# Performance work log

Hardware: AMD Instinct MI355X
Metric: run time of the kernel (lower is better)

The kernel has to match this reference:

```python
import jax, jax.numpy as jnp
import numpy as np

B, S, D, H = 2, 2048, 1024, 16
HD = D // H  # head_dim = 64


def setup_inputs() -> dict:
    key = jax.random.key(0)
    k1, k2, k3, k4, k5 = jax.random.split(key, 5)
    x = jax.random.normal(k1, (B, S, D), dtype=jnp.float32)
    # causal additive mask [S, S]: 0 on/below diagonal, -1e9 above
    mask = jnp.where(jnp.tril(jnp.ones((S, S), dtype=bool)), 0.0, -1e9).astype(jnp.float32)
    scale = 1.0 / np.sqrt(D)
    W_qkv = jax.random.normal(k2, (D, 3 * D), dtype=jnp.float32) * scale
    b_qkv = jax.random.normal(k3, (3 * D,), dtype=jnp.float32) * 0.01
    W_o = jax.random.normal(k4, (D, D), dtype=jnp.float32) * scale
    b_o = jax.random.normal(k5, (D,), dtype=jnp.float32) * 0.01
    return {"x": x, "mask": mask, "W_qkv": W_qkv, "b_qkv": b_qkv, "W_o": W_o, "b_o": b_o}


def reference(x, mask, W_qkv, b_qkv, W_o, b_o):
    b, s, d = x.shape
    qkv = x @ W_qkv + b_qkv                         # [B,S,3D]
    qkv = qkv.reshape(b, s, H, 3 * HD).transpose(0, 2, 1, 3)  # [B,H,S,3*HD]
    q, k, v = jnp.split(qkv, 3, axis=-1)            # each [B,H,S,HD]
    scores = jnp.einsum('bhqd,bhkd->bhqk', q, k) / np.sqrt(HD)  # [B,H,S,S]
    scores = scores + mask                           # broadcast [S,S] additive mask
    attn = jax.nn.softmax(scores, axis=-1)
    vals = jnp.einsum('bhqk,bhkd->bhqd', attn, v)    # [B,H,S,HD]
    vals = vals.transpose(0, 2, 1, 3).reshape(b, s, d)
    return vals @ W_o + b_o
```

## Files before the change

kernel.cpp:

```cpp
#include <hip/hip_runtime.h>

#define NB 2
#define NS 2048
#define ND 1024
#define NH 16
#define NHD 64
#define QLD (3 * ND)
#define PADP 72

typedef unsigned short u16;
typedef __attribute__((ext_vector_type(8))) short short8;
typedef __attribute__((ext_vector_type(4))) float f32x4;

__device__ __forceinline__ u16 f2b(float f) {
    unsigned int x = __float_as_uint(f);
    return (u16)((x + 0x7fffu + ((x >> 16) & 1u)) >> 16);
}

__device__ __forceinline__ unsigned int cvtpk(float lo, float hi) {
    unsigned int r;
    asm("v_cvt_pk_bf16_f32 %0, %1, %2" : "=v"(r) : "v"(lo), "v"(hi));
    return r;
}

__device__ __forceinline__ int swz8(int d) {
    return ((d >> 1) ^ (d >> 3)) & 7;
}

__global__ __launch_bounds__(256) void prep(
    const float* __restrict__ x, u16* __restrict__ x_bf,
    const float* __restrict__ Wqkv, u16* __restrict__ WqkvT,
    const float* __restrict__ Wo, u16* __restrict__ WoT)
{
    __shared__ u16 Ts[64 * 72];
    const int bid = blockIdx.x;
    const int t = threadIdx.x;

    if (bid < 2048) {
        const int i = (bid * 256 + t) * 8;
        float4 a = *(const float4*)(x + i);
        float4 b = *(const float4*)(x + i + 4);
        *(ushort4*)(x_bf + i)     = make_ushort4(f2b(a.x), f2b(a.y), f2b(a.z), f2b(a.w));
        *(ushort4*)(x_bf + i + 4) = make_ushort4(f2b(b.x), f2b(b.y), f2b(b.z), f2b(b.w));
        return;
    }

    const float* W; u16* WT; int N, bx, by;
    if (bid < 2048 + 768) {
        const int r = bid - 2048;
        W = Wqkv; WT = WqkvT; N = QLD; bx = r % 48; by = r / 48;
    } else {
        const int r = bid - 2816;
        W = Wo; WT = WoT; N = ND; bx = r & 15; by = r >> 4;
    }
    const int K = ND;
    const int k0 = by << 6, n0 = bx << 6;
    const int rr0 = t >> 4, c = (t & 15) << 2;
    #pragma unroll
    for (int rr = 0; rr < 64; rr += 16) {
        float4 v = *(const float4*)&W[(size_t)(k0 + rr0 + rr) * N + n0 + c];
        Ts[(c + 0) * 72 + rr0 + rr] = f2b(v.x);
        Ts[(c + 1) * 72 + rr0 + rr] = f2b(v.y);
        Ts[(c + 2) * 72 + rr0 + rr] = f2b(v.z);
        Ts[(c + 3) * 72 + rr0 + rr] = f2b(v.w);
    }
    __syncthreads();
    const int n = t >> 2, cc = (t & 3) << 4;
    uint4 a = *(const uint4*)&Ts[n * 72 + cc];
    uint4 b = *(const uint4*)&Ts[n * 72 + cc + 8];
    *(uint4*)&WT[(size_t)(n0 + n) * K + k0 + cc]     = a;
    *(uint4*)&WT[(size_t)(n0 + n) * K + k0 + cc + 8] = b;
}

template <int BN, bool STORE_BF16>
__global__ __launch_bounds__(256) void gemm_mfma(
    const u16* __restrict__ A, const u16* __restrict__ BT,
    const float* __restrict__ bias,
    void* __restrict__ C, int M, int N, int K)
{
    constexpr int AIS = 4;
    constexpr int BIS = BN / 32;
    constexpr int NJ  = BN / 32;
    __shared__ u16 As[128 * 64];
    __shared__ u16 Bs[BN * 64];

    const int tid = threadIdx.x;
    const int wave = tid >> 6, lane = tid & 63;
    const int col = lane & 15, quad = lane >> 4;
    const int wm = wave >> 1, wn = wave & 1;

    const int nwgx = gridDim.x;
    const int wg = blockIdx.y * nwgx + blockIdx.x;
    const int cpx = (nwgx * gridDim.y) >> 3;
    const int swz = (wg & 7) * cpx + (wg >> 3);
    const int row0 = (swz / nwgx) << 7, col0 = (swz % nwgx) * BN;

    f32x4 acc[4][NJ] = {};

    const u16* asrc[AIS];
    u16* adst[AIS];
    #pragma unroll
    for (int is = 0; is < AIS; ++is) {
        const int J = is * 256 + wave * 64 + lane;
        const int m = J >> 3;
        const int q = (J & 7) ^ swz8(m);
        asrc[is] = A + (size_t)(row0 + m) * K + q * 8;
        adst[is] = &As[(size_t)(is * 256 + wave * 64) * 8];
    }
    const u16* bsrc[BIS];
    u16* bdst[BIS];
    #pragma unroll
    for (int is = 0; is < BIS; ++is) {
        const int J = is * 256 + wave * 64 + lane;
        const int m = J >> 3;
        const int q = (J & 7) ^ swz8(m);
        bsrc[is] = BT + (size_t)(col0 + m) * K + q * 8;
        bdst[is] = &Bs[(size_t)(is * 256 + wave * 64) * 8];
    }

    for (int kk = 0; kk < K; kk += 64) {
        __syncthreads();
        #pragma unroll
        for (int is = 0; is < AIS; ++is)
            __builtin_amdgcn_global_load_lds(
                (const __attribute__((address_space(1))) unsigned int*)(asrc[is] + kk),
                (__attribute__((address_space(3))) unsigned int*)adst[is], 16, 0, 0);
        #pragma unroll
        for (int is = 0; is < BIS; ++is)
            __builtin_amdgcn_global_load_lds(
                (const __attribute__((address_space(1))) unsigned int*)(bsrc[is] + kk),
                (__attribute__((address_space(3))) unsigned int*)bdst[is], 16, 0, 0);
        __syncthreads();

        #pragma unroll
        for (int h = 0; h < 2; ++h) {
            short8 af[4], bf[NJ];
            #pragma unroll
            for (int i = 0; i < 4; ++i) {
                const int m = wm * 64 + i * 16 + col;
                af[i] = *(const short8*)&As[(m * 8 + ((4 * h + quad) ^ swz8(m))) * 8];
            }
            #pragma unroll
            for (int j = 0; j < NJ; ++j) {
                const int n = wn * (BN / 2) + j * 16 + col;
                bf[j] = *(const short8*)&Bs[(n * 8 + ((4 * h + quad) ^ swz8(n))) * 8];
            }
            #pragma unroll
            for (int i = 0; i < 4; ++i)
                #pragma unroll
                for (int j = 0; j < NJ; ++j)
                    acc[i][j] = __builtin_amdgcn_mfma_f32_16x16x32_bf16(
                        af[i], bf[j], acc[i][j], 0, 0, 0);
        }
    }

    #pragma unroll
    for (int j = 0; j < NJ; ++j) {
        const int gc = col0 + wn * (BN / 2) + j * 16 + col;
        const float bj = bias[gc];
        #pragma unroll
        for (int i = 0; i < 4; ++i) {
            const int gr = row0 + wm * 64 + i * 16 + quad * 4;
            #pragma unroll
            for (int r = 0; r < 4; ++r) {
                const float v = acc[i][j][r] + bj;
                if (STORE_BF16)
                    ((u16*)C)[(size_t)(gr + r) * N + gc] = f2b(v);
                else
                    ((float*)C)[(size_t)(gr + r) * N + gc] = v;
            }
        }
    }
}

__global__ __launch_bounds__(256) void attn_kernel(
    const u16* __restrict__ qkv, u16* __restrict__ vals)
{
    __shared__ u16 Ks[2][64 * 64];
    __shared__ u16 Vt[2][64 * 64];
    __shared__ u16 Ps[64 * PADP];

    const int tid = threadIdx.x;
    const int wave = tid >> 6, lane = tid & 63;
    const int col = lane & 15, quad = lane >> 4;
    const int qtA = blockIdx.x;
    const int qtB = 31 - qtA;
    const int bh = blockIdx.y;
    const int b = bh >> 4, h = bh & 15;
    const size_t base = (size_t)b * NS * QLD + (size_t)h * (3 * NHD);
    const int qloc = wave * 16 + col;

    int Jrow[2], Jcol[2];
    #pragma unroll
    for (int is = 0; is < 2; ++is) {
        const int J = is * 256 + wave * 64 + lane;
        Jrow[is] = J >> 3;
        Jcol[is] = ((J & 7) ^ (Jrow[is] & 7)) << 3;
    }

    auto stage_tile = [&](int buf, int srow, int coloff) {
        #pragma unroll
        for (int is = 0; is < 2; ++is) {
            __builtin_amdgcn_global_load_lds(
                (const __attribute__((address_space(1))) unsigned int*)
                    (qkv + base + (size_t)(srow + Jrow[is]) * QLD + coloff + Jcol[is]),
                (__attribute__((address_space(3))) unsigned int*)
                    &Ks[buf][(size_t)(is * 256 + wave * 64) * 8], 16, 0, 0);
        }
    };
    auto read_frag = [&](int buf, int row, int half) -> short8 {
        const int blk = row * 8 + ((quad + (half << 2)) ^ (row & 7));
        return *(const short8*)&Ks[buf][blk << 3];
    };

    const int vtx = tid & 15, vty = tid >> 4;
    const int vk0 = vty << 2, vd0 = vtx << 2;
    auto load_vregs = [&](int kt, ushort4* vr) {
        const u16* vsrc = qkv + base + (size_t)(kt * 64 + vk0) * QLD + 2 * NHD + vd0;
        vr[0] = *(const ushort4*)(vsrc);
        vr[1] = *(const ushort4*)(vsrc + QLD);
        vr[2] = *(const ushort4*)(vsrc + 2 * QLD);
        vr[3] = *(const ushort4*)(vsrc + 3 * QLD);
    };
    const int vC = vty >> 1, vS = (vty & 1) << 2;
    auto write_vt = [&](int buf, const ushort4* vr) {
        #pragma unroll
        for (int i = 0; i < 4; ++i) {
            const int d = vd0 + i;
            u16* p = &Vt[buf][d * 64 + ((vC ^ swz8(d)) << 3) + vS];
            *(ushort4*)p = make_ushort4(((const u16*)&vr[0])[i],
                                        ((const u16*)&vr[1])[i],
                                        ((const u16*)&vr[2])[i],
                                        ((const u16*)&vr[3])[i]);
        }
    };

    stage_tile(0, qtA * 64, 0);
    stage_tile(1, qtB * 64, 0);
    __syncthreads();
    short8 bqA0 = read_frag(0, qloc, 0), bqA1 = read_frag(0, qloc, 1);
    short8 bqB0 = read_frag(1, qloc, 0), bqB1 = read_frag(1, qloc, 1);
    __syncthreads();

    f32x4 accA[4] = {}, accB[4] = {};
    float mA = -1e30f, lA = 0.f, mB = -1e30f, lB = 0.f;

    auto qk = [&](const short8& b0, const short8& b1,
                  short8 (&kb)[4][2], f32x4 (&s)[4]) {
        __builtin_amdgcn_s_setprio(1);
        #pragma unroll
        for (int kg = 0; kg < 4; ++kg) {
            s[kg] = __builtin_amdgcn_mfma_f32_16x16x32_bf16(kb[kg][0], b0, s[kg], 0, 0, 0);
            s[kg] = __builtin_amdgcn_mfma_f32_16x16x32_bf16(kb[kg][1], b1, s[kg], 0, 0, 0);
        }
        __builtin_amdgcn_s_setprio(0);
    };

    auto sm = [&](f32x4 (&s)[4], f32x4 (&acc)[4], float& m, float& l, bool diag) {
        #pragma unroll
        for (int kg = 0; kg < 4; ++kg)
            #pragma unroll
            for (int r = 0; r < 4; ++r) {
                float v = s[kg][r] * 0.125f;
                if (diag && (kg * 16 + quad * 4 + r > qloc)) v = -1e30f;
                s[kg][r] = v;
            }
        float mx = -1e30f;
        #pragma unroll
        for (int kg = 0; kg < 4; ++kg)
            mx = fmaxf(mx, fmaxf(fmaxf(s[kg][0], s[kg][1]), fmaxf(s[kg][2], s[kg][3])));
        mx = fmaxf(mx, __shfl_xor(mx, 16, 64));
        mx = fmaxf(mx, __shfl_xor(mx, 32, 64));
        if (!__all(mx <= m + 8.f)) {
            const float mn = fmaxf(m, mx);
            const float alpha = __expf(m - mn);
            m = mn;
            l *= alpha;
            #pragma unroll
            for (int dg = 0; dg < 4; ++dg)
                #pragma unroll
                for (int r = 0; r < 4; ++r) acc[dg][r] *= alpha;
        }
        float psum = 0.f;
        #pragma unroll
        for (int kg = 0; kg < 4; ++kg) {
            float p0 = __expf(s[kg][0] - m);
            float p1 = __expf(s[kg][1] - m);
            float p2 = __expf(s[kg][2] - m);
            float p3 = __expf(s[kg][3] - m);
            psum += (p0 + p1) + (p2 + p3);
            uint2 w;
            w.x = cvtpk(p0, p1);
            w.y = cvtpk(p2, p3);
            *(uint2*)&Ps[qloc * PADP + kg * 16 + quad * 4] = w;
        }
        psum += __shfl_xor(psum, 16, 64);
        psum += __shfl_xor(psum, 32, 64);
        l += psum;
    };

    auto pv = [&](short8 (&vb)[4][2], f32x4 (&acc)[4]) {
        short8 pb0 = *(const short8*)&Ps[qloc * PADP + quad * 8];
        short8 pb1 = *(const short8*)&Ps[qloc * PADP + 32 + quad * 8];
        __builtin_amdgcn_s_setprio(1);
        #pragma unroll
        for (int dg = 0; dg < 4; ++dg) {
            acc[dg] = __builtin_amdgcn_mfma_f32_16x16x32_bf16(vb[dg][0], pb0, acc[dg], 0, 0, 0);
            acc[dg] = __builtin_amdgcn_mfma_f32_16x16x32_bf16(vb[dg][1], pb1, acc[dg], 0, 0, 0);
        }
        __builtin_amdgcn_s_setprio(0);
    };

    ushort4 vr[4];
    stage_tile(0, 0, NHD);
    load_vregs(0, vr);
    write_vt(0, vr);

    for (int kt = 0; kt <= qtB; ++kt) {
        const int cur = kt & 1, nxt = cur ^ 1;
        __syncthreads();
        if (kt < qtB) {
            stage_tile(nxt, (kt + 1) * 64, NHD);
            load_vregs(kt + 1, vr);
        }

        short8 kb[4][2], vb[4][2];
        #pragma unroll
        for (int kg = 0; kg < 4; ++kg) {
            kb[kg][0] = read_frag(cur, kg * 16 + col, 0);
            kb[kg][1] = read_frag(cur, kg * 16 + col, 1);
        }
        #pragma unroll
        for (int dg = 0; dg < 4; ++dg) {
            const int n = dg * 16 + col;
            #pragma unroll
            for (int c = 0; c < 2; ++c)
                vb[dg][c] = *(const short8*)
                    &Vt[cur][n * 64 + (((4 * c + quad) ^ swz8(n)) << 3)];
        }

        {
            f32x4 sB[4] = {};
            qk(bqB0, bqB1, kb, sB);
            sm(sB, accB, mB, lB, kt == qtB);
            if (kt <= qtA) {
                f32x4 sA[4] = {};
                qk(bqA0, bqA1, kb, sA);
                pv(vb, accB);
                sm(sA, accA, mA, lA, kt == qtA);
                pv(vb, accA);
            } else {
                pv(vb, accB);
            }
        }

        if (kt < qtB) write_vt(nxt, vr);
    }

    {
        const float inv = 1.f / lA;
        const size_t rowoff = ((size_t)b * NS + qtA * 64 + qloc) * ND + h * NHD;
        #pragma unroll
        for (int dg = 0; dg < 4; ++dg) {
            uint2 o;
            o.x = cvtpk(accA[dg][0] * inv, accA[dg][1] * inv);
            o.y = cvtpk(accA[dg][2] * inv, accA[dg][3] * inv);
            *(uint2*)(vals + rowoff + dg * 16 + quad * 4) = o;
        }
    }
    {
        const float inv = 1.f / lB;
        const size_t rowoff = ((size_t)b * NS + qtB * 64 + qloc) * ND + h * NHD;
        #pragma unroll
        for (int dg = 0; dg < 4; ++dg) {
            uint2 o;
            o.x = cvtpk(accB[dg][0] * inv, accB[dg][1] * inv);
            o.y = cvtpk(accB[dg][2] * inv, accB[dg][3] * inv);
            *(uint2*)(vals + rowoff + dg * 16 + quad * 4) = o;
        }
    }
}

extern "C" void kernel_launch(void* const* d_in, const int* in_sizes, int n_in,
                              void* d_out, int out_size, void* d_ws, size_t ws_size,
                              hipStream_t stream)
{
    const float* x    = (const float*)d_in[0];
    const float* Wqkv = (const float*)d_in[2];
    const float* bqkv = (const float*)d_in[3];
    const float* Wo   = (const float*)d_in[4];
    const float* bo   = (const float*)d_in[5];
    float* out = (float*)d_out;

    u16* x_bf   = (u16*)d_ws;
    u16* WqkvT  = x_bf   + (size_t)4096 * 1024;
    u16* WoT    = WqkvT  + (size_t)3072 * 1024;
    u16* qkv    = WoT    + (size_t)1024 * 1024;
    u16* vals   = qkv    + (size_t)4096 * 3072;

    const int M = NB * NS;

    prep<<<dim3(2048 + 768 + 256), dim3(256), 0, stream>>>(
        x, x_bf, Wqkv, WqkvT, Wo, WoT);

    gemm_mfma<128, true><<<dim3(QLD / 128, M / 128), dim3(256), 0, stream>>>(
        x_bf, WqkvT, bqkv, qkv, M, QLD, ND);
    attn_kernel<<<dim3(16, NB * NH), dim3(256), 0, stream>>>(qkv, vals);
    gemm_mfma<64, false><<<dim3(ND / 64, M / 128), dim3(256), 0, stream>>>(
        vals, WoT, bo, out, M, ND, ND);
}
```

Measured before the change: 216.8 us.

## Halve GEMM K-tile, parameterize BM, shrink output GEMM tile, serialize attention halves

The GEMM kernel now takes a BM template parameter and stages K in 32-wide chunks with a 4-slot XOR swizzle, halving shared memory per block. The output projection uses 64x64 tiles so its grid doubles in size. In the attention loop, the interleaved QK/softmax/PV of the two query tiles is split into two sequential blocks, which reduces live score registers. The trade-off is twice as many barrier-separated K iterations per GEMM and less interleaving of MFMA work with softmax in attention.

```diff
diff --git a/kernel.cpp b/kernel.cpp
--- a/kernel.cpp
+++ b/kernel.cpp
@@ -72,17 +72,18 @@
     *(uint4*)&WT[(size_t)(n0 + n) * K + k0 + cc + 8] = b;
 }
 
-template <int BN, bool STORE_BF16>
+template <int BM, int BN, bool STORE_BF16>
 __global__ __launch_bounds__(256) void gemm_mfma(
     const u16* __restrict__ A, const u16* __restrict__ BT,
     const float* __restrict__ bias,
     void* __restrict__ C, int M, int N, int K)
 {
-    constexpr int AIS = 4;
-    constexpr int BIS = BN / 32;
+    constexpr int AIS = BM / 64;
+    constexpr int BIS = BN / 64;
+    constexpr int MI  = BM / 32;
     constexpr int NJ  = BN / 32;
-    __shared__ u16 As[128 * 64];
-    __shared__ u16 Bs[BN * 64];
+    __shared__ u16 As[BM * 32];
+    __shared__ u16 Bs[BN * 32];
 
     const int tid = threadIdx.x;
     const int wave = tid >> 6, lane = tid & 63;
@@ -93,17 +94,17 @@
     const int wg = blockIdx.y * nwgx + blockIdx.x;
     const int cpx = (nwgx * gridDim.y) >> 3;
     const int swz = (wg & 7) * cpx + (wg >> 3);
-    const int row0 = (swz / nwgx) << 7, col0 = (swz % nwgx) * BN;
-
-    f32x4 acc[4][NJ] = {};
+    const int row0 = (swz / nwgx) * BM, col0 = (swz % nwgx) * BN;
+
+    f32x4 acc[MI][NJ] = {};
 
     const u16* asrc[AIS];
     u16* adst[AIS];
     #pragma unroll
     for (int is = 0; is < AIS; ++is) {
         const int J = is * 256 + wave * 64 + lane;
-        const int m = J >> 3;
-        const int q = (J & 7) ^ swz8(m);
+        const int m = J >> 2;
+        const int q = (J & 3) ^ ((m >> 1) & 3);
         asrc[is] = A + (size_t)(row0 + m) * K + q * 8;
         adst[is] = &As[(size_t)(is * 256 + wave * 64) * 8];
     }
@@ -112,13 +113,13 @@
     #pragma unroll
     for (int is = 0; is < BIS; ++is) {
         const int J = is * 256 + wave * 64 + lane;
-        const int m = J >> 3;
-        const int q = (J & 7) ^ swz8(m);
+        const int m = J >> 2;
+        const int q = (J & 3) ^ ((m >> 1) & 3);
         bsrc[is] = BT + (size_t)(col0 + m) * K + q * 8;
         bdst[is] = &Bs[(size_t)(is * 256 + wave * 64) * 8];
     }
 
-    for (int kk = 0; kk < K; kk += 64) {
+    for (int kk = 0; kk < K; kk += 32) {
         __syncthreads();
         #pragma unroll
         for (int is = 0; is < AIS; ++is)
@@ -132,26 +133,23 @@
                 (__attribute__((address_space(3))) unsigned int*)bdst[is], 16, 0, 0);
         __syncthreads();
 
-        #pragma unroll
-        for (int h = 0; h < 2; ++h) {
-            short8 af[4], bf[NJ];
+        short8 af[MI], bf[NJ];
+        #pragma unroll
+        for (int i = 0; i < MI; ++i) {
+            const int m = wm * (BM / 2) + i * 16 + col;
+            af[i] = *(const short8*)&As[(m * 4 + (quad ^ ((m >> 1) & 3))) * 8];
+        }
+        #pragma unroll
+        for (int j = 0; j < NJ; ++j) {
+            const int n = wn * (BN / 2) + j * 16 + col;
+            bf[j] = *(const short8*)&Bs[(n * 4 + (quad ^ ((n >> 1) & 3))) * 8];
+        }
+        #pragma unroll
+        for (int i = 0; i < MI; ++i)
             #pragma unroll
-            for (int i = 0; i < 4; ++i) {
-                const int m = wm * 64 + i * 16 + col;
-                af[i] = *(const short8*)&As[(m * 8 + ((4 * h + quad) ^ swz8(m))) * 8];
-            }
-            #pragma unroll
-            for (int j = 0; j < NJ; ++j) {
-                const int n = wn * (BN / 2) + j * 16 + col;
-                bf[j] = *(const short8*)&Bs[(n * 8 + ((4 * h + quad) ^ swz8(n))) * 8];
-            }
-            #pragma unroll
-            for (int i = 0; i < 4; ++i)
-                #pragma unroll
-                for (int j = 0; j < NJ; ++j)
-                    acc[i][j] = __builtin_amdgcn_mfma_f32_16x16x32_bf16(
-                        af[i], bf[j], acc[i][j], 0, 0, 0);
-        }
+            for (int j = 0; j < NJ; ++j)
+                acc[i][j] = __builtin_amdgcn_mfma_f32_16x16x32_bf16(
+                    af[i], bf[j], acc[i][j], 0, 0, 0);
     }
 
     #pragma unroll
@@ -159,8 +157,8 @@
         const int gc = col0 + wn * (BN / 2) + j * 16 + col;
         const float bj = bias[gc];
         #pragma unroll
-        for (int i = 0; i < 4; ++i) {
-            const int gr = row0 + wm * 64 + i * 16 + quad * 4;
+        for (int i = 0; i < MI; ++i) {
+            const int gr = row0 + wm * (BM / 2) + i * 16 + quad * 4;
             #pragma unroll
             for (int r = 0; r < 4; ++r) {
                 const float v = acc[i][j][r] + bj;
@@ -340,18 +338,16 @@
         }
 
         {
-            f32x4 sB[4] = {};
-            qk(bqB0, bqB1, kb, sB);
-            sm(sB, accB, mB, lB, kt == qtB);
-            if (kt <= qtA) {
-                f32x4 sA[4] = {};
-                qk(bqA0, bqA1, kb, sA);
-                pv(vb, accB);
-                sm(sA, accA, mA, lA, kt == qtA);
-                pv(vb, accA);
-            } else {
-                pv(vb, accB);
-            }
+            f32x4 s[4] = {};
+            qk(bqB0, bqB1, kb, s);
+            sm(s, accB, mB, lB, kt == qtB);
+            pv(vb, accB);
+        }
+        if (kt <= qtA) {
+            f32x4 s[4] = {};
+            qk(bqA0, bqA1, kb, s);
+            sm(s, accA, mA, lA, kt == qtA);
+            pv(vb, accA);
         }
 
         if (kt < qtB) write_vt(nxt, vr);
@@ -403,9 +399,9 @@
     prep<<<dim3(2048 + 768 + 256), dim3(256), 0, stream>>>(
         x, x_bf, Wqkv, WqkvT, Wo, WoT);
 
-    gemm_mfma<128, true><<<dim3(QLD / 128, M / 128), dim3(256), 0, stream>>>(
+    gemm_mfma<128, 128, true><<<dim3(QLD / 128, M / 128), dim3(256), 0, stream>>>(
         x_bf, WqkvT, bqkv, qkv, M, QLD, ND);
     attn_kernel<<<dim3(16, NB * NH), dim3(256), 0, stream>>>(qkv, vals);
-    gemm_mfma<64, false><<<dim3(ND / 64, M / 128), dim3(256), 0, stream>>>(
+    gemm_mfma<64, 64, false><<<dim3(ND / 64, M / 64), dim3(256), 0, stream>>>(
         vals, WoT, bo, out, M, ND, ND);
 }
```

New measurement: 202.6 us. 6.6% less time.
